# Kernel optimization log

Hardware: AMD Instinct MI355X
Metric: run time of the kernel (lower is better)

## Reference

```python
import jax, jax.numpy as jnp
import numpy as np
import math

EMBED_DIM = 768
HIDDEN_DIM = 96
N_HEAD = 8
BATCH = 32
K_LEN = 512
Q_LEN = 512


def setup_inputs() -> dict:
    key = jax.random.key(0)
    k1, k2, k3, k4 = jax.random.split(key, 4)
    k = jax.random.normal(k1, (BATCH, K_LEN, EMBED_DIM), dtype=jnp.float32)
    q = jax.random.normal(k2, (BATCH, Q_LEN, EMBED_DIM), dtype=jnp.float32)
    # per-head projection weights, as in nn.Parameter(torch.FloatTensor(n_head, embed_dim, hidden_dim))
    w_kx = jax.random.normal(k3, (N_HEAD, EMBED_DIM, HIDDEN_DIM), dtype=jnp.float32) * (1.0 / math.sqrt(EMBED_DIM))
    w_qx = jax.random.normal(k4, (N_HEAD, EMBED_DIM, HIDDEN_DIM), dtype=jnp.float32) * (1.0 / math.sqrt(EMBED_DIM))
    return {"k": k, "q": q, "w_kx": w_kx, "w_qx": w_qx}


def reference(k, q, w_kx, w_qx):
    # scaled_dot_product variant of ABSA-PyTorch Attention.
    mb, k_len, _ = k.shape
    q_len = q.shape[1]
    hidden = w_kx.shape[-1]
    # per-head projections: [h, b, len, d]  (torch: repeat over heads + bmm)
    kx = jnp.einsum('bke,hed->hbkd', k, w_kx)
    qx = jnp.einsum('bqe,hed->hbqd', q, w_qx)
    # scores [h, b, q, k], scaled
    score = jnp.einsum('hbqd,hbkd->hbqk', qx, kx) / jnp.sqrt(jnp.asarray(hidden, kx.dtype))
    attn = jax.nn.softmax(score, axis=-1)
    # weighted sum over the PROJECTED keys (kx), as in the original: bmm(score, kx)
    out = jnp.einsum('hbqk,hbkd->hbqd', attn, kx)
    # torch.cat(torch.split(output, mb, dim=0), dim=-1): concat heads on last dim
    out = jnp.transpose(out, (1, 2, 0, 3)).reshape(mb, q_len, w_kx.shape[0] * hidden)
    return out
```

## Files before the change

### kernel.cpp

```cpp
#include <hip/hip_runtime.h>
#include <hip/hip_bf16.h>

typedef short short8 __attribute__((ext_vector_type(8)));
typedef float floatx4 __attribute__((ext_vector_type(4)));

#define EMB 768
#define DH 96
#define NHEAD 8
#define NBATCH 32
#define SEQ 512
#define MROWS (NBATCH * SEQ)

__device__ __forceinline__ unsigned short f2bf(float x) {
    __hip_bfloat16 h = __float2bfloat16(x);
    union { __hip_bfloat16 b; unsigned short u; } c;
    c.b = h;
    return c.u;
}

__global__ __launch_bounds__(256) void cvt_w_kernel(
    const float* __restrict__ wk, const float* __restrict__ wq,
    unsigned short* __restrict__ wtk, unsigned short* __restrict__ wtq)
{
    __shared__ float ws[64][97];
    const int h = blockIdx.x, et = blockIdx.y;
    const float* wsrc = (blockIdx.z ? wq : wk) + (size_t)h * EMB * DH;
    unsigned short* o = blockIdx.z ? wtq : wtk;
    const int t = threadIdx.x;
    const int e0 = et * 64;
    #pragma unroll
    for (int i = 0; i < 6; ++i) {
        int f = i * 256 + t;
        int e = f / 24, c = f % 24;
        float4 v = *(const float4*)(wsrc + (size_t)(e0 + e) * DH + c * 4);
        ws[e][c*4+0] = v.x; ws[e][c*4+1] = v.y; ws[e][c*4+2] = v.z; ws[e][c*4+3] = v.w;
    }
    __syncthreads();
    #pragma unroll
    for (int i = 0; i < 3; ++i) {
        int f = i * 256 + t;
        int d = f >> 3, c8 = f & 7;
        short8 v;
        #pragma unroll
        for (int j = 0; j < 8; ++j) v[j] = (short)f2bf(ws[c8*8+j][d]);
        *(short8*)(o + (size_t)(h*DH + d) * EMB + e0 + c8*8) = v;
    }
}

__global__ __launch_bounds__(256, 2) void proj_kernel(
    const float* __restrict__ x,
    const unsigned short* __restrict__ wt,
    unsigned short* __restrict__ xp)
{
    __shared__ char As[16384];
    __shared__ char Bs[32768];
    const int t = threadIdx.x;
    const int wv = t >> 6, l = t & 63;
    const int lr = l & 15, lg = l >> 4, l7 = l & 7;
    const int mt = blockIdx.x * 128, nt = blockIdx.y * 256;
    const int mw = (wv >> 1) * 64, nw = (wv & 1) * 128;

    floatx4 acc[4][8];
    #pragma unroll
    for (int a = 0; a < 4; ++a)
        #pragma unroll
        for (int b = 0; b < 8; ++b) acc[a][b] = (floatx4){0.f, 0.f, 0.f, 0.f};

    for (int kt = 0; kt < EMB / 64; ++kt) {
        __syncthreads();
        #pragma unroll
        for (int i = 0; i < 4; ++i) {
            int f = i * 256 + t;
            int row = f >> 3, s = f & 7;
            const float* xs = x + (size_t)(mt + row) * EMB + kt*64 + s*8;
            float4 ga = *(const float4*)xs;
            float4 gb = *(const float4*)(xs + 4);
            union { unsigned short h[8]; short8 s8; } pk;
            pk.h[0] = f2bf(ga.x); pk.h[1] = f2bf(ga.y);
            pk.h[2] = f2bf(ga.z); pk.h[3] = f2bf(ga.w);
            pk.h[4] = f2bf(gb.x); pk.h[5] = f2bf(gb.y);
            pk.h[6] = f2bf(gb.z); pk.h[7] = f2bf(gb.w);
            *(short8*)(As + row*128 + ((s ^ (row & 7)) * 16)) = pk.s8;
        }
        #pragma unroll
        for (int i = 0; i < 8; ++i) {
            int f = i * 256 + t;
            int row = f >> 3, s = f & 7;
            short8 gw = *(const short8*)(wt + (size_t)(nt + row) * EMB + kt*64 + s*8);
            *(short8*)(Bs + row*128 + ((s ^ (row & 7)) * 16)) = gw;
        }
        __syncthreads();
        #pragma unroll
        for (int ks = 0; ks < 2; ++ks) {
            const int sl = (ks*4 + lg) ^ l7;
            short8 af[4], bf[8];
            #pragma unroll
            for (int mf = 0; mf < 4; ++mf)
                af[mf] = *(const short8*)(As + (mw + 16*mf + lr) * 128 + sl*16);
            #pragma unroll
            for (int nf = 0; nf < 8; ++nf)
                bf[nf] = *(const short8*)(Bs + (nw + 16*nf + lr) * 128 + sl*16);
            #pragma unroll
            for (int mf = 0; mf < 4; ++mf)
                #pragma unroll
                for (int nf = 0; nf < 8; ++nf)
                    acc[mf][nf] = __builtin_amdgcn_mfma_f32_16x16x32_bf16(
                        af[mf], bf[nf], acc[mf][nf], 0, 0, 0);
        }
    }
    #pragma unroll
    for (int mf = 0; mf < 4; ++mf)
        #pragma unroll
        for (int r = 0; r < 4; ++r) {
            int m = mt + mw + 16*mf + lg*4 + r;
            unsigned short* op = xp + (size_t)m * EMB + nt + nw + lr;
            #pragma unroll
            for (int nf = 0; nf < 8; ++nf) op[16*nf] = f2bf(acc[mf][nf][r]);
        }
}

__global__ __launch_bounds__(256) void attn_kernel(
    const unsigned short* __restrict__ kx,
    const unsigned short* __restrict__ qx,
    float* __restrict__ out)
{
    __shared__ char Ks[64 * 192];
    __shared__ char Kt[96 * 128];
    __shared__ char Ps[128 * 128];
    const int t = threadIdx.x;
    const int wv = t >> 6, l = t & 63;
    const int lr = l & 15, lg = l >> 4, l7 = l & 7;
    const int q0 = blockIdx.x * 128, b = blockIdx.y, h = blockIdx.z;
    const size_t bq = (size_t)b * SEQ;
    const int hcol = h * DH;
    const float scale = 0.10206207261596575f;

    short8 qf[2][3];
    #pragma unroll
    for (int mf = 0; mf < 2; ++mf)
        #pragma unroll
        for (int ks = 0; ks < 3; ++ks)
            qf[mf][ks] = *(const short8*)(qx
                + (bq + q0 + 32*wv + 16*mf + lr) * EMB + hcol + ks*32 + lg*8);

    floatx4 oacc[2][6];
    #pragma unroll
    for (int mf = 0; mf < 2; ++mf)
        #pragma unroll
        for (int nf = 0; nf < 6; ++nf) oacc[mf][nf] = (floatx4){0.f, 0.f, 0.f, 0.f};
    float lsum[2][4];
    #pragma unroll
    for (int mf = 0; mf < 2; ++mf)
        #pragma unroll
        for (int r = 0; r < 4; ++r) lsum[mf][r] = 0.f;

    for (int kt = 0; kt < SEQ / 64; ++kt) {
        __syncthreads();
        #pragma unroll
        for (int i = 0; i < 2; ++i) {
            int f = i * 256 + t;
            if (f < 384) {
                int rp = f / 12, s = f - rp * 12;
                int r0 = rp * 2;
                const unsigned short* src = kx + (bq + kt*64 + r0) * EMB + hcol + s*8;
                short8 g0 = *(const short8*)src;
                short8 g1 = *(const short8*)(src + EMB);
                *(short8*)(Ks + r0*192 + ((s + r0) % 12) * 16) = g0;
                *(short8*)(Ks + (r0+1)*192 + ((s + r0 + 1) % 12) * 16) = g1;
                #pragma unroll
                for (int j = 0; j < 8; ++j) {
                    int d = s*8 + j;
                    unsigned int pr = (unsigned int)(unsigned short)g0[j]
                                    | ((unsigned int)(unsigned short)g1[j] << 16);
                    *(unsigned int*)(Kt + d*128
                        + (((r0 >> 3) ^ (d & 7) ^ ((d >> 3) & 7)) * 16)
                        + (r0 & 7) * 2) = pr;
                }
            }
        }
        __syncthreads();

        floatx4 sf[2][4];
        #pragma unroll
        for (int mf = 0; mf < 2; ++mf)
            #pragma unroll
            for (int nf = 0; nf < 4; ++nf) sf[mf][nf] = (floatx4){0.f, 0.f, 0.f, 0.f};
        #pragma unroll
        for (int ks = 0; ks < 3; ++ks) {
            short8 bk[4];
            #pragma unroll
            for (int nf = 0; nf < 4; ++nf) {
                int row = 16*nf + lr;
                bk[nf] = *(const short8*)(Ks + row*192 + ((ks*4 + lg + row) % 12) * 16);
            }
            #pragma unroll
            for (int mf = 0; mf < 2; ++mf)
                #pragma unroll
                for (int nf = 0; nf < 4; ++nf)
                    sf[mf][nf] = __builtin_amdgcn_mfma_f32_16x16x32_bf16(
                        qf[mf][ks], bk[nf], sf[mf][nf], 0, 0, 0);
        }

        #pragma unroll
        for (int mf = 0; mf < 2; ++mf)
            #pragma unroll
            for (int nf = 0; nf < 4; ++nf)
                #pragma unroll
                for (int r = 0; r < 4; ++r) {
                    float p = __expf(fmaf(sf[mf][nf][r], scale, -12.0f));
                    lsum[mf][r] += p;
                    int qrow = 32*wv + 16*mf + lg*4 + r;
                    int kcol = 16*nf + lr;
                    *(unsigned short*)(Ps + qrow*128
                        + (((kcol >> 3) ^ (qrow & 7)) * 16) + (kcol & 7) * 2) = f2bf(p);
                }

        #pragma unroll
        for (int ks2 = 0; ks2 < 2; ++ks2) {
            short8 ap[2];
            #pragma unroll
            for (int mf = 0; mf < 2; ++mf) {
                int row = 32*wv + 16*mf + lr;
                int sl = (ks2*4 + lg) ^ (row & 7);
                ap[mf] = *(const short8*)(Ps + row*128 + sl*16);
            }
            short8 bv[6];
            #pragma unroll
            for (int nf = 0; nf < 6; ++nf) {
                int d = 16*nf + lr;
                int sl2 = (ks2*4 + lg) ^ (d & 7) ^ ((d >> 3) & 7);
                bv[nf] = *(const short8*)(Kt + d*128 + sl2*16);
            }
            #pragma unroll
            for (int mf = 0; mf < 2; ++mf)
                #pragma unroll
                for (int nf = 0; nf < 6; ++nf)
                    oacc[mf][nf] = __builtin_amdgcn_mfma_f32_16x16x32_bf16(
                        ap[mf], bv[nf], oacc[mf][nf], 0, 0, 0);
        }
    }

    float inv[2][4];
    #pragma unroll
    for (int mf = 0; mf < 2; ++mf)
        #pragma unroll
        for (int r = 0; r < 4; ++r) {
            float v = lsum[mf][r];
            v += __shfl_xor(v, 1);
            v += __shfl_xor(v, 2);
            v += __shfl_xor(v, 4);
            v += __shfl_xor(v, 8);
            inv[mf][r] = 1.0f / v;
        }
    #pragma unroll
    for (int mf = 0; mf < 2; ++mf)
        #pragma unroll
        for (int r = 0; r < 4; ++r) {
            int q = q0 + 32*wv + 16*mf + lg*4 + r;
            float* op = out + (bq + q) * (NHEAD*DH) + hcol + lr;
            #pragma unroll
            for (int nf = 0; nf < 6; ++nf) op[16*nf] = oacc[mf][nf][r] * inv[mf][r];
        }
}

extern "C" void kernel_launch(void* const* d_in, const int* in_sizes, int n_in,
                              void* d_out, int out_size, void* d_ws, size_t ws_size,
                              hipStream_t stream) {
    const float* kin = (const float*)d_in[0];
    const float* qin = (const float*)d_in[1];
    const float* wk  = (const float*)d_in[2];
    const float* wq  = (const float*)d_in[3];
    float* out = (float*)d_out;

    unsigned short* wsu = (unsigned short*)d_ws;
    const size_t SZX = (size_t)MROWS * EMB;
    unsigned short* kxb = wsu;
    unsigned short* qxb = wsu + SZX;
    unsigned short* wtk = wsu + 2*SZX;
    unsigned short* wtq = wtk + (size_t)EMB * (NHEAD*DH);

    cvt_w_kernel<<<dim3(NHEAD, EMB/64, 2), 256, 0, stream>>>(wk, wq, wtk, wtq);
    proj_kernel<<<dim3(MROWS/128, (NHEAD*DH)/256), 256, 0, stream>>>(kin, wtk, kxb);
    proj_kernel<<<dim3(MROWS/128, (NHEAD*DH)/256), 256, 0, stream>>>(qin, wtq, qxb);
    attn_kernel<<<dim3(SEQ/128, NBATCH, NHEAD), 256, 0, stream>>>(kxb, qxb, out);
}
```

Before: 125.0 us.

## Keep softmax probabilities in registers via transposed score MFMA, drop P LDS staging

Swaps the MFMA operand order for the score product so each lane holds scores for one query row across several keys. Those values can then be converted to bf16 directly into the A operand of the PV MFMA, removing the shared-memory round trip for the probability tile. The transposed K buffer gets a new chunked, XOR-swizzled layout read as two 4-element halves, and the row-sum reduction and normalization are reworked to match the new lane mapping. This saves LDS traffic and space at the cost of extra in-register packing and shuffles.

```diff
diff --git a/kernel.cpp b/kernel.cpp
--- a/kernel.cpp
+++ b/kernel.cpp
@@ -2,6 +2,7 @@
 #include <hip/hip_bf16.h>
 
 typedef short short8 __attribute__((ext_vector_type(8)));
+typedef short short4v __attribute__((ext_vector_type(4)));
 typedef float floatx4 __attribute__((ext_vector_type(4)));
 
 #define EMB 768
@@ -125,11 +126,10 @@
     float* __restrict__ out)
 {
     __shared__ char Ks[64 * 192];
-    __shared__ char Kt[96 * 128];
-    __shared__ char Ps[128 * 128];
+    __shared__ char Kt2[16 * 768];
     const int t = threadIdx.x;
     const int wv = t >> 6, l = t & 63;
-    const int lr = l & 15, lg = l >> 4, l7 = l & 7;
+    const int lr = l & 15, lg = l >> 4;
     const int q0 = blockIdx.x * 128, b = blockIdx.y, h = blockIdx.z;
     const size_t bq = (size_t)b * SEQ;
     const int hcol = h * DH;
@@ -143,16 +143,12 @@
             qf[mf][ks] = *(const short8*)(qx
                 + (bq + q0 + 32*wv + 16*mf + lr) * EMB + hcol + ks*32 + lg*8);
 
-    floatx4 oacc[2][6];
+    floatx4 of[2][6];
     #pragma unroll
     for (int mf = 0; mf < 2; ++mf)
         #pragma unroll
-        for (int nf = 0; nf < 6; ++nf) oacc[mf][nf] = (floatx4){0.f, 0.f, 0.f, 0.f};
-    float lsum[2][4];
-    #pragma unroll
-    for (int mf = 0; mf < 2; ++mf)
-        #pragma unroll
-        for (int r = 0; r < 4; ++r) lsum[mf][r] = 0.f;
+        for (int dt = 0; dt < 6; ++dt) of[mf][dt] = (floatx4){0.f, 0.f, 0.f, 0.f};
+    float lsum[2] = {0.f, 0.f};
 
     for (int kt = 0; kt < SEQ / 64; ++kt) {
         __syncthreads();
@@ -167,14 +163,14 @@
                 short8 g1 = *(const short8*)(src + EMB);
                 *(short8*)(Ks + r0*192 + ((s + r0) % 12) * 16) = g0;
                 *(short8*)(Ks + (r0+1)*192 + ((s + r0 + 1) % 12) * 16) = g1;
+                const int c = rp >> 1, tau = 5 * (c & 3);
+                char* kb = Kt2 + c*768 + ((rp & 1) << 2);
                 #pragma unroll
                 for (int j = 0; j < 8; ++j) {
                     int d = s*8 + j;
                     unsigned int pr = (unsigned int)(unsigned short)g0[j]
                                     | ((unsigned int)(unsigned short)g1[j] << 16);
-                    *(unsigned int*)(Kt + d*128
-                        + (((r0 >> 3) ^ (d & 7) ^ ((d >> 3) & 7)) * 16)
-                        + (r0 & 7) * 2) = pr;
+                    *(unsigned int*)(kb + ((d ^ tau) << 3)) = pr;
                 }
             }
         }
@@ -198,7 +194,7 @@
                 #pragma unroll
                 for (int nf = 0; nf < 4; ++nf)
                     sf[mf][nf] = __builtin_amdgcn_mfma_f32_16x16x32_bf16(
-                        qf[mf][ks], bk[nf], sf[mf][nf], 0, 0, 0);
+                        bk[nf], qf[mf][ks], sf[mf][nf], 0, 0, 0);
         }
 
         #pragma unroll
@@ -208,58 +204,53 @@
                 #pragma unroll
                 for (int r = 0; r < 4; ++r) {
                     float p = __expf(fmaf(sf[mf][nf][r], scale, -12.0f));
-                    lsum[mf][r] += p;
-                    int qrow = 32*wv + 16*mf + lg*4 + r;
-                    int kcol = 16*nf + lr;
-                    *(unsigned short*)(Ps + qrow*128
-                        + (((kcol >> 3) ^ (qrow & 7)) * 16) + (kcol & 7) * 2) = f2bf(p);
+                    sf[mf][nf][r] = p;
+                    lsum[mf] += p;
                 }
 
         #pragma unroll
         for (int ks2 = 0; ks2 < 2; ++ks2) {
-            short8 ap[2];
-            #pragma unroll
-            for (int mf = 0; mf < 2; ++mf) {
-                int row = 32*wv + 16*mf + lr;
-                int sl = (ks2*4 + lg) ^ (row & 7);
-                ap[mf] = *(const short8*)(Ps + row*128 + sl*16);
+            union { unsigned short hsh[8]; short8 s8; } ap[2];
+            #pragma unroll
+            for (int mf = 0; mf < 2; ++mf)
+                #pragma unroll
+                for (int j = 0; j < 8; ++j)
+                    ap[mf].hsh[j] = f2bf(sf[mf][2*ks2 + (j >> 2)][j & 3]);
+            const int cbase = (8*ks2 + lg) * 768;
+            const int tau = 5 * lg;
+            #pragma unroll
+            for (int dt = 0; dt < 6; ++dt) {
+                const int gofs = ((16*dt + lr) ^ tau) << 3;
+                short4v lo = *(const short4v*)(Kt2 + cbase + gofs);
+                short4v hi = *(const short4v*)(Kt2 + cbase + 3072 + gofs);
+                short8 bv;
+                bv[0] = lo[0]; bv[1] = lo[1]; bv[2] = lo[2]; bv[3] = lo[3];
+                bv[4] = hi[0]; bv[5] = hi[1]; bv[6] = hi[2]; bv[7] = hi[3];
+                #pragma unroll
+                for (int mf = 0; mf < 2; ++mf)
+                    of[mf][dt] = __builtin_amdgcn_mfma_f32_16x16x32_bf16(
+                        ap[mf].s8, bv, of[mf][dt], 0, 0, 0);
             }
-            short8 bv[6];
-            #pragma unroll
-            for (int nf = 0; nf < 6; ++nf) {
-                int d = 16*nf + lr;
-                int sl2 = (ks2*4 + lg) ^ (d & 7) ^ ((d >> 3) & 7);
-                bv[nf] = *(const short8*)(Kt + d*128 + sl2*16);
-            }
-            #pragma unroll
-            for (int mf = 0; mf < 2; ++mf)
-                #pragma unroll
-                for (int nf = 0; nf < 6; ++nf)
-                    oacc[mf][nf] = __builtin_amdgcn_mfma_f32_16x16x32_bf16(
-                        ap[mf], bv[nf], oacc[mf][nf], 0, 0, 0);
-        }
-    }
-
-    float inv[2][4];
+        }
+    }
+
+    float invq[2];
+    #pragma unroll
+    for (int mf = 0; mf < 2; ++mf) {
+        float v = lsum[mf];
+        v += __shfl_xor(v, 16);
+        v += __shfl_xor(v, 32);
+        invq[mf] = 1.0f / v;
+    }
     #pragma unroll
     for (int mf = 0; mf < 2; ++mf)
         #pragma unroll
         for (int r = 0; r < 4; ++r) {
-            float v = lsum[mf][r];
-            v += __shfl_xor(v, 1);
-            v += __shfl_xor(v, 2);
-            v += __shfl_xor(v, 4);
-            v += __shfl_xor(v, 8);
-            inv[mf][r] = 1.0f / v;
-        }
-    #pragma unroll
-    for (int mf = 0; mf < 2; ++mf)
-        #pragma unroll
-        for (int r = 0; r < 4; ++r) {
-            int q = q0 + 32*wv + 16*mf + lg*4 + r;
+            float inv = __shfl(invq[mf], 4*lg + r);
+            int q = q0 + 32*wv + 16*mf + 4*lg + r;
             float* op = out + (bq + q) * (NHEAD*DH) + hcol + lr;
             #pragma unroll
-            for (int nf = 0; nf < 6; ++nf) op[16*nf] = oacc[mf][nf][r] * inv[mf][r];
+            for (int dt = 0; dt < 6; ++dt) op[16*dt] = of[mf][dt][r] * inv;
         }
 }
 
```

After: 120.1 us. 3.9% less time.
